# Kernel tuning notes

Hardware: AMD Instinct MI355X
Metric: run time of the kernel (lower is better)

The kernel has to match this reference:

```python
import jax, jax.numpy as jnp
import numpy as np

N, E, D, L = 50000, 800000, 128, 3
BN_EPS = 1e-5

def setup_inputs() -> dict:
    key = jax.random.key(0)
    ks = jax.random.split(key, 6)
    x = jax.random.normal(ks[0], (N, D), dtype=jnp.float32)
    edge_index = jax.random.randint(ks[1], (2, E), 0, N, dtype=jnp.int64)
    W1 = jax.random.normal(ks[2], (L, D, D), dtype=jnp.float32) * (1.0 / np.sqrt(D))
    W2 = jax.random.normal(ks[3], (L, D, D), dtype=jnp.float32) * (1.0 / np.sqrt(D))
    return {
        'x': x, 'edge_index': edge_index,
        'W1': W1, 'b1': jnp.zeros((L, D), jnp.float32),
        'gamma': jnp.ones((L, D), jnp.float32), 'beta': jnp.zeros((L, D), jnp.float32),
        'bn_mean': jnp.zeros((L, D), jnp.float32), 'bn_var': jnp.ones((L, D), jnp.float32),
        'W2': W2, 'b2': jnp.zeros((L, D), jnp.float32),
        'eps': jnp.zeros((L,), jnp.float32),
    }

def reference(x, edge_index, W1, b1, gamma, beta, bn_mean, bn_var, W2, b2, eps):
    src, dst = edge_index[0], edge_index[1]
    h = x
    for l in range(L):
        # GIN aggregation: (1+eps)*h_i + sum_{j->i} h_j  (scatter-add over edges)
        agg = jax.ops.segment_sum(h[src], dst, num_segments=N)  # [N, D]
        z = (1.0 + eps[l]) * h + agg
        # MLP: Linear -> BatchNorm(eval, running stats) -> ReLU -> Linear
        z = z @ W1[l] + b1[l]
        z = (z - bn_mean[l]) * jax.lax.rsqrt(bn_var[l] + BN_EPS) * gamma[l] + beta[l]
        z = jax.nn.relu(z)
        z = z @ W2[l] + b2[l]
        if l < L - 1:
            z = jax.nn.relu(z)  # inter-layer ReLU; dropout is identity in eval
        h = z
    return h
```

## Files before the change

kernel.cpp:

```cpp
#include <hip/hip_runtime.h>
#include <hip/hip_fp16.h>

#define NN 50000
#define NE 800000
#define DD 128
#define NL 3
#define BN_EPS 1e-5f

typedef short bf16x8 __attribute__((ext_vector_type(8)));
typedef float f32x4  __attribute__((ext_vector_type(4)));
typedef unsigned int u32x4 __attribute__((ext_vector_type(4)));


__device__ __forceinline__ unsigned int rne16(float v) {
    unsigned int u = __float_as_uint(v);
    return (u + 0x7fffu + ((u >> 16) & 1u)) >> 16;
}
__device__ __forceinline__ unsigned int packf(float v) {
    unsigned int hb = rne16(v);
    float hf = __uint_as_float(hb << 16);
    unsigned int lb = rne16(v - hf);
    return (hb << 16) | lb;
}
__device__ __forceinline__ float unpackf(unsigned int p) {
    return __uint_as_float(p & 0xffff0000u) + __uint_as_float(p << 16);
}


#define ET (NE / 4)

__global__ void hist_kernel(const int* __restrict__ dst, int* __restrict__ counts) {
    int t = blockIdx.x * 256 + threadIdx.x;
    if (t >= ET) return;
    int d0 = dst[t], d1 = dst[t + ET], d2 = dst[t + 2 * ET], d3 = dst[t + 3 * ET];
    atomicAdd(&counts[d0], 1);
    atomicAdd(&counts[d1], 1);
    atomicAdd(&counts[d2], 1);
    atomicAdd(&counts[d3], 1);
}

__global__ void scan1_kernel(const int* __restrict__ counts, int* __restrict__ otmp,
                             int* __restrict__ bsums) {
    __shared__ int sd[1024];
    int t = threadIdx.x;
    int i = blockIdx.x * 1024 + t;
    int v = (i < NN) ? counts[i] : 0;
    sd[t] = v; __syncthreads();
    for (int off = 1; off < 1024; off <<= 1) {
        int tmp = (t >= off) ? sd[t - off] : 0;
        __syncthreads();
        sd[t] += tmp;
        __syncthreads();
    }
    if (i < NN) otmp[i] = sd[t] - v;
    if (t == 1023) bsums[blockIdx.x] = sd[1023];
}

__global__ void scan2_kernel(const int* __restrict__ bsums, int* __restrict__ boffs, int nb) {
    __shared__ int sd[64];
    int t = threadIdx.x;
    int v = (t < nb) ? bsums[t] : 0;
    sd[t] = v; __syncthreads();
    for (int off = 1; off < 64; off <<= 1) {
        int tmp = (t >= off) ? sd[t - off] : 0;
        __syncthreads();
        sd[t] += tmp;
        __syncthreads();
    }
    if (t < nb) boffs[t] = sd[t] - v;
}

__global__ void scan3_kernel(const int* __restrict__ otmp, const int* __restrict__ boffs,
                             int* __restrict__ offsets) {
    int i = blockIdx.x * 1024 + threadIdx.x;
    if (i < NN) offsets[i] = otmp[i] + boffs[blockIdx.x];
}

__global__ void fill_kernel(const int* __restrict__ src, const int* __restrict__ dst,
                            const int* __restrict__ offsets, int* __restrict__ cursor,
                            int* __restrict__ csr) {
    int t = blockIdx.x * 256 + threadIdx.x;
    if (t >= ET) return;
    int d[4], s[4], p[4];
#pragma unroll
    for (int q = 0; q < 4; ++q) {
        d[q] = dst[t + q * ET];
        s[q] = src[t + q * ET];
    }
#pragma unroll
    for (int q = 0; q < 4; ++q)
        p[q] = offsets[d[q]] + atomicAdd(&cursor[d[q]], 1);
#pragma unroll
    for (int q = 0; q < 4; ++q)
        csr[p[q]] = s[q];
}


__global__ void wsplit_kernel(const float* __restrict__ W1, const float* __restrict__ W2,
                              unsigned short* __restrict__ Whi, unsigned short* __restrict__ Wlo) {
    int idx = blockIdx.x * 256 + threadIdx.x;
    if (idx >= 6 * 16384) return;
    int m = idx >> 14;
    int r = idx & 16383;
    int n = r >> 7, k = r & 127;
    const float* Wsrc = (m < 3) ? (W1 + (size_t)m * 16384) : (W2 + (size_t)(m - 3) * 16384);
    float v = Wsrc[k * DD + n];
    unsigned int hb = rne16(v);
    float hf = __uint_as_float(hb << 16);
    unsigned int lb = rne16(v - hf);
    Whi[idx] = (unsigned short)hb;
    Wlo[idx] = (unsigned short)lb;
}


__global__ void tofp16_kernel(const float* __restrict__ x, unsigned int* __restrict__ x16) {
    int i = blockIdx.x * 256 + threadIdx.x;
    if (i >= NN * 64) return;
    float2 v = ((const float2*)x)[i];
    __half2 h = __float22half2_rn(v);
    x16[i] = __builtin_bit_cast(unsigned int, h);
}


template <bool SELF_F32>
__global__ __launch_bounds__(256) void agg_kernel(const void* __restrict__ selfv,
    const unsigned int* __restrict__ h16,
    const int* __restrict__ offsets, const int* __restrict__ counts,
    const int* __restrict__ csr, const float* __restrict__ eps, int l,
    unsigned int* __restrict__ aggp) {
    int wid = (int)((blockIdx.x * 256 + threadIdx.x) >> 6);
    int lane = threadIdx.x & 63;
    if (wid >= NN) return;
    float se = 1.0f + eps[l];
    float ax, ay;
    if (SELF_F32) {
        float2 s = ((const float2*)((const float*)selfv + (size_t)wid * DD))[lane];
        ax = s.x * se; ay = s.y * se;
    } else {
        uint2 s = ((const uint2*)((const unsigned int*)selfv + (size_t)wid * DD))[lane];
        ax = unpackf(s.x) * se; ay = unpackf(s.y) * se;
    }
    int e = offsets[wid];
    int end = e + counts[wid];
    for (; e + 8 <= end; e += 8) {
        int idx[8];
#pragma unroll
        for (int q = 0; q < 8; ++q) idx[q] = csr[e + q];
        unsigned int p[8];
#pragma unroll
        for (int q = 0; q < 8; ++q) p[q] = h16[(size_t)idx[q] * 64 + lane];
#pragma unroll
        for (int q = 0; q < 8; ++q) {
            float2 f = __half22float2(__builtin_bit_cast(__half2, p[q]));
            ax += f.x; ay += f.y;
        }
    }
    for (; e < end; ++e) {
        unsigned int p = h16[(size_t)csr[e] * 64 + lane];
        float2 f = __half22float2(__builtin_bit_cast(__half2, p));
        ax += f.x; ay += f.y;
    }
    uint2 o; o.x = packf(ax); o.y = packf(ay);
    ((uint2*)(aggp + (size_t)wid * DD))[lane] = o;
}


__device__ __forceinline__ void gemm_half(const unsigned int* Al, const bf16x8 (&wh)[4][2],
                                          const bf16x8 (&wl)[4][2], int lane,
                                          f32x4 (&acc)[4][2]) {
#pragma unroll
    for (int r = 0; r < 4; ++r) {
        int rl = r * 16 + (lane & 15);
        int sw = rl & 7;
#pragma unroll
        for (int kb = 0; kb < 4; ++kb) {
            int c0 = kb * 8 + ((lane >> 4) << 1);
            u32x4 q0 = *(const u32x4*)(&Al[rl * DD + ((c0 ^ sw) << 2)]);
            u32x4 q1 = *(const u32x4*)(&Al[rl * DD + (((c0 + 1) ^ sw) << 2)]);
            u32x4 hr, lr;
            hr.x = (q0.x >> 16) | (q0.y & 0xffff0000u);
            hr.y = (q0.z >> 16) | (q0.w & 0xffff0000u);
            hr.z = (q1.x >> 16) | (q1.y & 0xffff0000u);
            hr.w = (q1.z >> 16) | (q1.w & 0xffff0000u);
            lr.x = (q0.x & 0xffffu) | (q0.y << 16);
            lr.y = (q0.z & 0xffffu) | (q0.w << 16);
            lr.z = (q1.x & 0xffffu) | (q1.y << 16);
            lr.w = (q1.z & 0xffffu) | (q1.w << 16);
            bf16x8 ah = __builtin_bit_cast(bf16x8, hr);
            bf16x8 al = __builtin_bit_cast(bf16x8, lr);
#pragma unroll
            for (int nb = 0; nb < 2; ++nb) {
                acc[r][nb] = __builtin_amdgcn_mfma_f32_16x16x32_bf16(ah, wh[kb][nb], acc[r][nb], 0, 0, 0);
                acc[r][nb] = __builtin_amdgcn_mfma_f32_16x16x32_bf16(ah, wl[kb][nb], acc[r][nb], 0, 0, 0);
                acc[r][nb] = __builtin_amdgcn_mfma_f32_16x16x32_bf16(al, wh[kb][nb], acc[r][nb], 0, 0, 0);
            }
        }
    }
}

__global__ __launch_bounds__(256, 3) void mlp_kernel(
    const unsigned int* __restrict__ Ap,
    const unsigned short* __restrict__ Wh1, const unsigned short* __restrict__ Wl1,
    const unsigned short* __restrict__ Wh2, const unsigned short* __restrict__ Wl2,
    const float* __restrict__ b1v, const float* __restrict__ gamma,
    const float* __restrict__ beta, const float* __restrict__ mean,
    const float* __restrict__ var, const float* __restrict__ b2v,
    void* __restrict__ outp, unsigned short* __restrict__ out16, int last) {
    __shared__ unsigned int Al[64 * DD];
    int t = threadIdx.x;
    int lane = t & 63, w = t >> 6;
    int r0 = blockIdx.x * 64;
    int cb = w * 32;
    int nfrag = lane & 15;
    int kfrag = (lane >> 4) << 3;

    bf16x8 wh[4][2], wl[4][2];
#pragma unroll
    for (int kb = 0; kb < 4; ++kb)
#pragma unroll
        for (int nb = 0; nb < 2; ++nb) {
            size_t off = (size_t)(cb + nb * 16 + nfrag) * DD + kb * 32 + kfrag;
            wh[kb][nb] = *(const bf16x8*)(Wh1 + off);
            wl[kb][nb] = *(const bf16x8*)(Wl1 + off);
        }

    {
        int cchunk = t & 31;
#pragma unroll
        for (int it = 0; it < 8; ++it) {
            int rl = it * 8 + (t >> 5);
            int rg = r0 + rl; if (rg > NN - 1) rg = NN - 1;
            u32x4 v = *(const u32x4*)(Ap + (size_t)rg * DD + cchunk * 4);
            *(u32x4*)(&Al[rl * DD + ((cchunk ^ (rl & 7)) << 2)]) = v;
        }
    }
    __syncthreads();

    f32x4 acc[4][2];
#pragma unroll
    for (int r = 0; r < 4; ++r)
#pragma unroll
        for (int nb = 0; nb < 2; ++nb) acc[r][nb] = (f32x4){0.f, 0.f, 0.f, 0.f};

    gemm_half(Al, wh, wl, lane, acc);

#pragma unroll
    for (int kb = 0; kb < 4; ++kb)
#pragma unroll
        for (int nb = 0; nb < 2; ++nb) {
            size_t off = (size_t)(cb + nb * 16 + nfrag) * DD + kb * 32 + kfrag;
            wh[kb][nb] = *(const bf16x8*)(Wh2 + off);
            wl[kb][nb] = *(const bf16x8*)(Wl2 + off);
        }

    __syncthreads();

#pragma unroll
    for (int nb = 0; nb < 2; ++nb) {
        int col = cb + nb * 16 + nfrag;
        float bs = b1v[col];
        float iv = rsqrtf(var[col] + BN_EPS);
        float sc = iv * gamma[col];
        float sh = beta[col] - mean[col] * sc;
#pragma unroll
        for (int r = 0; r < 4; ++r)
#pragma unroll
            for (int j = 0; j < 4; ++j) {
                int row = r * 16 + ((lane >> 4) << 2) + j;
                float v = fmaxf(fmaf(acc[r][nb][j] + bs, sc, sh), 0.0f);
                Al[row * DD + ((((col >> 2) ^ (row & 7)) << 2) | (col & 3))] = packf(v);
            }
    }
    __syncthreads();

#pragma unroll
    for (int r = 0; r < 4; ++r)
#pragma unroll
        for (int nb = 0; nb < 2; ++nb) acc[r][nb] = (f32x4){0.f, 0.f, 0.f, 0.f};

    gemm_half(Al, wh, wl, lane, acc);

#pragma unroll
    for (int nb = 0; nb < 2; ++nb) {
        int col = cb + nb * 16 + nfrag;
        float bs = b2v[col];
#pragma unroll
        for (int r = 0; r < 4; ++r)
#pragma unroll
            for (int j = 0; j < 4; ++j) {
                int orow = r0 + r * 16 + ((lane >> 4) << 2) + j;
                if (orow < NN) {
                    float v = acc[r][nb][j] + bs;
                    if (last) {
                        ((float*)outp)[(size_t)orow * DD + col] = v;
                    } else {
                        v = fmaxf(v, 0.0f);
                        ((unsigned int*)outp)[(size_t)orow * DD + col] = packf(v);
                        out16[(size_t)orow * DD + col] =
                            __builtin_bit_cast(unsigned short, __float2half_rn(v));
                    }
                }
            }
    }
}


extern "C" void kernel_launch(void* const* d_in, const int* in_sizes, int n_in,
                              void* d_out, int out_size, void* d_ws, size_t ws_size,
                              hipStream_t stream) {
    const float* x     = (const float*)d_in[0];
    const int*   eidx  = (const int*)d_in[1];
    const float* W1    = (const float*)d_in[2];
    const float* b1    = (const float*)d_in[3];
    const float* gamma = (const float*)d_in[4];
    const float* beta  = (const float*)d_in[5];
    const float* bnm   = (const float*)d_in[6];
    const float* bnv   = (const float*)d_in[7];
    const float* W2    = (const float*)d_in[8];
    const float* b2    = (const float*)d_in[9];
    const float* eps   = (const float*)d_in[10];
    float* out = (float*)d_out;

    const int* src = eidx;
    const int* dst = eidx + NE;

    char* wsp = (char*)d_ws;
    unsigned int* bufA = (unsigned int*)wsp;  wsp += (size_t)NN * DD * 4;
    unsigned int* bufB = (unsigned int*)wsp;  wsp += (size_t)NN * DD * 4;
    unsigned int* x16  = (unsigned int*)wsp;  wsp += (size_t)NN * DD * 2;
    unsigned int* h16  = (unsigned int*)wsp;  wsp += (size_t)NN * DD * 2;
    int* csr    = (int*)wsp;                  wsp += (size_t)NE * 4;
    int* counts = (int*)wsp;                  wsp += (size_t)NN * 4;
    int* offs   = (int*)wsp;                  wsp += (size_t)NN * 4;
    int* cursor = (int*)wsp;                  wsp += (size_t)NN * 4;
    unsigned short* Whi = (unsigned short*)wsp; wsp += (size_t)6 * 16384 * 2;
    unsigned short* Wlo = (unsigned short*)wsp; wsp += (size_t)6 * 16384 * 2;
    int* bsums  = (int*)wsp;                  wsp += 64 * 4;
    int* boffs  = (int*)wsp;                  wsp += 64 * 4;

    hipMemsetAsync(counts, 0, (size_t)NN * 4, stream);
    hipMemsetAsync(cursor, 0, (size_t)NN * 4, stream);

    int nbScan = (NN + 1023) / 1024;
    hist_kernel<<<(ET + 255) / 256, 256, 0, stream>>>(dst, counts);
    wsplit_kernel<<<(6 * 16384 + 255) / 256, 256, 0, stream>>>(W1, W2, Whi, Wlo);
    tofp16_kernel<<<(NN * 64 + 255) / 256, 256, 0, stream>>>(x, x16);
    scan1_kernel<<<nbScan, 1024, 0, stream>>>(counts, offs, bsums);
    scan2_kernel<<<1, 64, 0, stream>>>(bsums, boffs, nbScan);
    scan3_kernel<<<nbScan, 1024, 0, stream>>>(offs, boffs, offs);
    fill_kernel<<<(ET + 255) / 256, 256, 0, stream>>>(src, dst, offs, cursor, csr);

    int aggBlocks = (NN * 64 + 255) / 256;
    int gemmBlocks = (NN + 63) / 64;

    for (int l = 0; l < NL; ++l) {
        if (l == 0)
            agg_kernel<true><<<aggBlocks, 256, 0, stream>>>(x, x16, offs, counts, csr, eps, l, bufA);
        else
            agg_kernel<false><<<aggBlocks, 256, 0, stream>>>(bufB, h16, offs, counts, csr, eps, l, bufA);
        int last = (l == NL - 1);
        mlp_kernel<<<gemmBlocks, 256, 0, stream>>>(
            bufA,
            Whi + (size_t)l * 16384, Wlo + (size_t)l * 16384,
            Whi + (size_t)(3 + l) * 16384, Wlo + (size_t)(3 + l) * 16384,
            b1 + (size_t)l * DD, gamma + (size_t)l * DD, beta + (size_t)l * DD,
            bnm + (size_t)l * DD, bnv + (size_t)l * DD, b2 + (size_t)l * DD,
            last ? (void*)out : (void*)bufB, (unsigned short*)h16, last);
    }
}
```

Before: 419.8 us.

## Fuse neighbor aggregation into MLP kernel and build CSR via binned scatter

Aggregation is moved into the MLP kernel: each wave gathers neighbors for its rows and writes the packed sum straight into the shared-memory A tile. This removes the global round trip of the aggregate buffer and one launch per layer. CSR construction switches from global per-node atomics to a two-pass bin scatter that uses shared-memory atomics and per-bin fill. Double-buffered fp16 outputs are added so a layer never reads the feature copy it is writing. The risks are lower gather parallelism per block while its MFMA work waits, and a fixed bin capacity (BCAP) that could overflow on skewed degree distributions.

```diff
diff --git a/kernel.cpp b/kernel.cpp
--- a/kernel.cpp
+++ b/kernel.cpp
@@ -7,6 +7,11 @@
 #define NL 3
 #define BN_EPS 1e-5f
 
+#define NBIN 196
+#define BCAP 5120
+#define EB 4096
+#define NB3 ((NE + EB - 1) / EB)
+
 typedef short bf16x8 __attribute__((ext_vector_type(8)));
 typedef float f32x4  __attribute__((ext_vector_type(4)));
 typedef unsigned int u32x4 __attribute__((ext_vector_type(4)));
@@ -27,16 +32,53 @@
 }
 
 
-#define ET (NE / 4)
-
-__global__ void hist_kernel(const int* __restrict__ dst, int* __restrict__ counts) {
-    int t = blockIdx.x * 256 + threadIdx.x;
-    if (t >= ET) return;
-    int d0 = dst[t], d1 = dst[t + ET], d2 = dst[t + 2 * ET], d3 = dst[t + 3 * ET];
-    atomicAdd(&counts[d0], 1);
-    atomicAdd(&counts[d1], 1);
-    atomicAdd(&counts[d2], 1);
-    atomicAdd(&counts[d3], 1);
+__global__ __launch_bounds__(256) void binscatter_kernel(
+    const int* __restrict__ src, const int* __restrict__ dst,
+    int* __restrict__ bin_cursor, uint2* __restrict__ binned) {
+    __shared__ int lhist[NBIN];
+    __shared__ int lbase[NBIN];
+    __shared__ int lcur[NBIN];
+    int t = threadIdx.x;
+    for (int i = t; i < NBIN; i += 256) { lhist[i] = 0; lcur[i] = 0; }
+    __syncthreads();
+    int base = blockIdx.x * EB;
+    int d[16], s[16], b[16];
+#pragma unroll
+    for (int i = 0; i < 16; ++i) {
+        int e = base + t + i * 256;
+        if (e < NE) {
+            d[i] = dst[e]; s[i] = src[e]; b[i] = d[i] >> 8;
+            atomicAdd(&lhist[b[i]], 1);
+        } else b[i] = -1;
+    }
+    __syncthreads();
+    for (int i = t; i < NBIN; i += 256) {
+        int c = lhist[i];
+        lbase[i] = c ? atomicAdd(&bin_cursor[i], c) : 0;
+    }
+    __syncthreads();
+#pragma unroll
+    for (int i = 0; i < 16; ++i)
+        if (b[i] >= 0) {
+            int p = lbase[b[i]] + atomicAdd(&lcur[b[i]], 1);
+            binned[(size_t)b[i] * BCAP + p] = make_uint2((unsigned)s[i], (unsigned)d[i]);
+        }
+}
+
+__global__ __launch_bounds__(256) void bincount_kernel(
+    const uint2* __restrict__ binned, const int* __restrict__ bin_cursor,
+    int* __restrict__ counts) {
+    __shared__ int lcnt[256];
+    int bI = blockIdx.x, t = threadIdx.x;
+    lcnt[t] = 0;
+    __syncthreads();
+    int cnt = bin_cursor[bI];
+    const uint2* be = binned + (size_t)bI * BCAP;
+    for (int i = t; i < cnt; i += 256)
+        atomicAdd(&lcnt[be[i].y & 255], 1);
+    __syncthreads();
+    int node = bI * 256 + t;
+    if (node < NN) counts[node] = lcnt[t];
 }
 
 __global__ void scan1_kernel(const int* __restrict__ counts, int* __restrict__ otmp,
@@ -76,23 +118,21 @@
     if (i < NN) offsets[i] = otmp[i] + boffs[blockIdx.x];
 }
 
-__global__ void fill_kernel(const int* __restrict__ src, const int* __restrict__ dst,
-                            const int* __restrict__ offsets, int* __restrict__ cursor,
-                            int* __restrict__ csr) {
-    int t = blockIdx.x * 256 + threadIdx.x;
-    if (t >= ET) return;
-    int d[4], s[4], p[4];
-#pragma unroll
-    for (int q = 0; q < 4; ++q) {
-        d[q] = dst[t + q * ET];
-        s[q] = src[t + q * ET];
-    }
-#pragma unroll
-    for (int q = 0; q < 4; ++q)
-        p[q] = offsets[d[q]] + atomicAdd(&cursor[d[q]], 1);
-#pragma unroll
-    for (int q = 0; q < 4; ++q)
-        csr[p[q]] = s[q];
+__global__ __launch_bounds__(256) void binfill_kernel(
+    const uint2* __restrict__ binned, const int* __restrict__ bin_cursor,
+    const int* __restrict__ offs, int* __restrict__ csr) {
+    __shared__ int lcur[256];
+    int bI = blockIdx.x, t = threadIdx.x;
+    lcur[t] = 0;
+    __syncthreads();
+    int cnt = bin_cursor[bI];
+    const uint2* be = binned + (size_t)bI * BCAP;
+    for (int i = t; i < cnt; i += 256) {
+        uint2 e = be[i];
+        int node = (int)e.y;
+        int p = atomicAdd(&lcur[node & 255], 1);
+        csr[offs[node] + p] = (int)e.x;
+    }
 }
 
 
@@ -119,49 +159,6 @@
     float2 v = ((const float2*)x)[i];
     __half2 h = __float22half2_rn(v);
     x16[i] = __builtin_bit_cast(unsigned int, h);
-}
-
-
-template <bool SELF_F32>
-__global__ __launch_bounds__(256) void agg_kernel(const void* __restrict__ selfv,
-    const unsigned int* __restrict__ h16,
-    const int* __restrict__ offsets, const int* __restrict__ counts,
-    const int* __restrict__ csr, const float* __restrict__ eps, int l,
-    unsigned int* __restrict__ aggp) {
-    int wid = (int)((blockIdx.x * 256 + threadIdx.x) >> 6);
-    int lane = threadIdx.x & 63;
-    if (wid >= NN) return;
-    float se = 1.0f + eps[l];
-    float ax, ay;
-    if (SELF_F32) {
-        float2 s = ((const float2*)((const float*)selfv + (size_t)wid * DD))[lane];
-        ax = s.x * se; ay = s.y * se;
-    } else {
-        uint2 s = ((const uint2*)((const unsigned int*)selfv + (size_t)wid * DD))[lane];
-        ax = unpackf(s.x) * se; ay = unpackf(s.y) * se;
-    }
-    int e = offsets[wid];
-    int end = e + counts[wid];
-    for (; e + 8 <= end; e += 8) {
-        int idx[8];
-#pragma unroll
-        for (int q = 0; q < 8; ++q) idx[q] = csr[e + q];
-        unsigned int p[8];
-#pragma unroll
-        for (int q = 0; q < 8; ++q) p[q] = h16[(size_t)idx[q] * 64 + lane];
-#pragma unroll
-        for (int q = 0; q < 8; ++q) {
-            float2 f = __half22float2(__builtin_bit_cast(__half2, p[q]));
-            ax += f.x; ay += f.y;
-        }
-    }
-    for (; e < end; ++e) {
-        unsigned int p = h16[(size_t)csr[e] * 64 + lane];
-        float2 f = __half22float2(__builtin_bit_cast(__half2, p));
-        ax += f.x; ay += f.y;
-    }
-    uint2 o; o.x = packf(ax); o.y = packf(ay);
-    ((uint2*)(aggp + (size_t)wid * DD))[lane] = o;
 }
 
 
@@ -198,14 +195,17 @@
     }
 }
 
-__global__ __launch_bounds__(256, 3) void mlp_kernel(
-    const unsigned int* __restrict__ Ap,
+template <bool SELF_F32, bool LAST>
+__global__ __launch_bounds__(256, 3) void gin_layer_kernel(
+    const void* __restrict__ selfv, const unsigned int* __restrict__ nbr16,
+    const int* __restrict__ offs, const int* __restrict__ counts,
+    const int* __restrict__ csr, const float* __restrict__ epsv, int l,
     const unsigned short* __restrict__ Wh1, const unsigned short* __restrict__ Wl1,
     const unsigned short* __restrict__ Wh2, const unsigned short* __restrict__ Wl2,
     const float* __restrict__ b1v, const float* __restrict__ gamma,
     const float* __restrict__ beta, const float* __restrict__ mean,
     const float* __restrict__ var, const float* __restrict__ b2v,
-    void* __restrict__ outp, unsigned short* __restrict__ out16, int last) {
+    void* __restrict__ outp, unsigned short* __restrict__ out16) {
     __shared__ unsigned int Al[64 * DD];
     int t = threadIdx.x;
     int lane = t & 63, w = t >> 6;
@@ -224,15 +224,40 @@
             wl[kb][nb] = *(const bf16x8*)(Wl1 + off);
         }
 
-    {
-        int cchunk = t & 31;
-#pragma unroll
-        for (int it = 0; it < 8; ++it) {
-            int rl = it * 8 + (t >> 5);
-            int rg = r0 + rl; if (rg > NN - 1) rg = NN - 1;
-            u32x4 v = *(const u32x4*)(Ap + (size_t)rg * DD + cchunk * 4);
-            *(u32x4*)(&Al[rl * DD + ((cchunk ^ (rl & 7)) << 2)]) = v;
-        }
+    float se = 1.0f + epsv[l];
+    for (int rr = w; rr < 64; rr += 4) {
+        int node = r0 + rr;
+        if (node >= NN) continue;
+        float ax, ay;
+        if (SELF_F32) {
+            float2 s = ((const float2*)((const float*)selfv + (size_t)node * DD))[lane];
+            ax = s.x * se; ay = s.y * se;
+        } else {
+            uint2 s = ((const uint2*)((const unsigned int*)selfv + (size_t)node * DD))[lane];
+            ax = unpackf(s.x) * se; ay = unpackf(s.y) * se;
+        }
+        int e = offs[node];
+        int end = e + counts[node];
+        for (; e + 8 <= end; e += 8) {
+            int idx[8];
+#pragma unroll
+            for (int q = 0; q < 8; ++q) idx[q] = csr[e + q];
+            unsigned int p[8];
+#pragma unroll
+            for (int q = 0; q < 8; ++q) p[q] = nbr16[(size_t)idx[q] * 64 + lane];
+#pragma unroll
+            for (int q = 0; q < 8; ++q) {
+                float2 f = __half22float2(__builtin_bit_cast(__half2, p[q]));
+                ax += f.x; ay += f.y;
+            }
+        }
+        for (; e < end; ++e) {
+            unsigned int p = nbr16[(size_t)csr[e] * 64 + lane];
+            float2 f = __half22float2(__builtin_bit_cast(__half2, p));
+            ax += f.x; ay += f.y;
+        }
+        uint2 o; o.x = packf(ax); o.y = packf(ay);
+        *(uint2*)(&Al[rr * DD + (((lane >> 1) ^ (rr & 7)) << 2) + ((lane & 1) << 1)]) = o;
     }
     __syncthreads();
 
@@ -291,7 +316,7 @@
                 int orow = r0 + r * 16 + ((lane >> 4) << 2) + j;
                 if (orow < NN) {
                     float v = acc[r][nb][j] + bs;
-                    if (last) {
+                    if (LAST) {
                         ((float*)outp)[(size_t)orow * DD + col] = v;
                     } else {
                         v = fmaxf(v, 0.0f);
@@ -325,46 +350,49 @@
     const int* dst = eidx + NE;
 
     char* wsp = (char*)d_ws;
-    unsigned int* bufA = (unsigned int*)wsp;  wsp += (size_t)NN * DD * 4;
-    unsigned int* bufB = (unsigned int*)wsp;  wsp += (size_t)NN * DD * 4;
+    unsigned int* pk0  = (unsigned int*)wsp;  wsp += (size_t)NN * DD * 4;
+    unsigned int* pk1  = (unsigned int*)wsp;  wsp += (size_t)NN * DD * 4;
     unsigned int* x16  = (unsigned int*)wsp;  wsp += (size_t)NN * DD * 2;
-    unsigned int* h16  = (unsigned int*)wsp;  wsp += (size_t)NN * DD * 2;
+    unsigned int* g16a = (unsigned int*)wsp;  wsp += (size_t)NN * DD * 2;
+    unsigned int* g16b = (unsigned int*)wsp;  wsp += (size_t)NN * DD * 2;
+    uint2* binned      = (uint2*)wsp;         wsp += (size_t)NBIN * BCAP * 8;
     int* csr    = (int*)wsp;                  wsp += (size_t)NE * 4;
     int* counts = (int*)wsp;                  wsp += (size_t)NN * 4;
     int* offs   = (int*)wsp;                  wsp += (size_t)NN * 4;
-    int* cursor = (int*)wsp;                  wsp += (size_t)NN * 4;
+    int* bin_cursor = (int*)wsp;              wsp += (size_t)NBIN * 4;
     unsigned short* Whi = (unsigned short*)wsp; wsp += (size_t)6 * 16384 * 2;
     unsigned short* Wlo = (unsigned short*)wsp; wsp += (size_t)6 * 16384 * 2;
     int* bsums  = (int*)wsp;                  wsp += 64 * 4;
     int* boffs  = (int*)wsp;                  wsp += 64 * 4;
 
-    hipMemsetAsync(counts, 0, (size_t)NN * 4, stream);
-    hipMemsetAsync(cursor, 0, (size_t)NN * 4, stream);
-
-    int nbScan = (NN + 1023) / 1024;
-    hist_kernel<<<(ET + 255) / 256, 256, 0, stream>>>(dst, counts);
+    hipMemsetAsync(bin_cursor, 0, (size_t)NBIN * 4, stream);
+
     wsplit_kernel<<<(6 * 16384 + 255) / 256, 256, 0, stream>>>(W1, W2, Whi, Wlo);
     tofp16_kernel<<<(NN * 64 + 255) / 256, 256, 0, stream>>>(x, x16);
+
+    int nbScan = (NN + 1023) / 1024;
+    binscatter_kernel<<<NB3, 256, 0, stream>>>(src, dst, bin_cursor, binned);
+    bincount_kernel<<<NBIN, 256, 0, stream>>>(binned, bin_cursor, counts);
     scan1_kernel<<<nbScan, 1024, 0, stream>>>(counts, offs, bsums);
     scan2_kernel<<<1, 64, 0, stream>>>(bsums, boffs, nbScan);
     scan3_kernel<<<nbScan, 1024, 0, stream>>>(offs, boffs, offs);
-    fill_kernel<<<(ET + 255) / 256, 256, 0, stream>>>(src, dst, offs, cursor, csr);
-
-    int aggBlocks = (NN * 64 + 255) / 256;
-    int gemmBlocks = (NN + 63) / 64;
-
-    for (int l = 0; l < NL; ++l) {
-        if (l == 0)
-            agg_kernel<true><<<aggBlocks, 256, 0, stream>>>(x, x16, offs, counts, csr, eps, l, bufA);
-        else
-            agg_kernel<false><<<aggBlocks, 256, 0, stream>>>(bufB, h16, offs, counts, csr, eps, l, bufA);
-        int last = (l == NL - 1);
-        mlp_kernel<<<gemmBlocks, 256, 0, stream>>>(
-            bufA,
-            Whi + (size_t)l * 16384, Wlo + (size_t)l * 16384,
-            Whi + (size_t)(3 + l) * 16384, Wlo + (size_t)(3 + l) * 16384,
-            b1 + (size_t)l * DD, gamma + (size_t)l * DD, beta + (size_t)l * DD,
-            bnm + (size_t)l * DD, bnv + (size_t)l * DD, b2 + (size_t)l * DD,
-            last ? (void*)out : (void*)bufB, (unsigned short*)h16, last);
-    }
-}
+    binfill_kernel<<<NBIN, 256, 0, stream>>>(binned, bin_cursor, offs, csr);
+
+    int layerBlocks = (NN + 63) / 64;
+
+    gin_layer_kernel<true, false><<<layerBlocks, 256, 0, stream>>>(
+        x, x16, offs, counts, csr, eps, 0,
+        Whi + 0 * 16384, Wlo + 0 * 16384, Whi + 3 * 16384, Wlo + 3 * 16384,
+        b1 + 0 * DD, gamma + 0 * DD, beta + 0 * DD, bnm + 0 * DD, bnv + 0 * DD, b2 + 0 * DD,
+        pk0, (unsigned short*)g16a);
+    gin_layer_kernel<false, false><<<layerBlocks, 256, 0, stream>>>(
+        pk0, g16a, offs, counts, csr, eps, 1,
+        Whi + 1 * 16384, Wlo + 1 * 16384, Whi + 4 * 16384, Wlo + 4 * 16384,
+        b1 + 1 * DD, gamma + 1 * DD, beta + 1 * DD, bnm + 1 * DD, bnv + 1 * DD, b2 + 1 * DD,
+        pk1, (unsigned short*)g16b);
+    gin_layer_kernel<false, true><<<layerBlocks, 256, 0, stream>>>(
+        pk1, g16b, offs, counts, csr, eps, 2,
+        Whi + 2 * 16384, Wlo + 2 * 16384, Whi + 5 * 16384, Wlo + 5 * 16384,
+        b1 + 2 * DD, gamma + 2 * DD, beta + 2 * DD, bnm + 2 * DD, bnv + 2 * DD, b2 + 2 * DD,
+        out, nullptr);
+}
```

Result: slower. 551.9 us (+31.5%).
